# Optimization experiments

Measured on AMD Instinct MI355X. Metric: run time of the kernel, lower is better.

Reference implementation:

```python
import jax, jax.numpy as jnp
import numpy as np
import math

B, S, HID, NH = 64, 512, 256, 4
DH = HID // NH
EPS = 1e-12


def _dense(x, W, b):
    # torch nn.Linear: y = x @ W.T + b, W: [out, in]
    return jnp.einsum('bsi,oi->bso', x, W) + b


def _heads(x):
    # [B,S,HID] -> [B,NH,S,DH]
    return x.reshape(B, S, NH, DH).transpose(0, 2, 1, 3)


def _layernorm(x, w, b):
    u = jnp.mean(x, -1, keepdims=True)
    s = jnp.mean((x - u) ** 2, -1, keepdims=True)
    return w * ((x - u) / jnp.sqrt(s + EPS)) + b


def _wasserstein(mq, cq, mk, ck):
    # mean part: ||mq||^2 + ||mk||^2 - 2 mq.mk
    m_ret = (-2.0 * jnp.einsum('bhqd,bhkd->bhqk', mq, mk)
             + jnp.sum(mq ** 2, -1, keepdims=True)
             + jnp.sum(mk ** 2, -1, keepdims=True).swapaxes(-1, -2))
    sq, sk = jnp.sqrt(jnp.clip(cq, 1e-24)), jnp.sqrt(jnp.clip(ck, 1e-24))
    c_ret = (-2.0 * jnp.einsum('bhqd,bhkd->bhqk', sq, sk)
             + jnp.sum(cq, -1, keepdims=True)
             + jnp.sum(ck, -1, keepdims=True).swapaxes(-1, -2))
    return m_ret + c_ret


def setup_inputs() -> dict:
    key = jax.random.key(0)
    ks = jax.random.split(key, 16)
    inp = {
        'input_mean': jax.random.normal(ks[0], (B, S, HID), jnp.float32),
        'input_cov': jax.random.normal(ks[1], (B, S, HID), jnp.float32),
        'attention_mask': jnp.zeros((B, 1, S, S), jnp.float32),
    }
    sc = 1.0 / math.sqrt(HID)
    names = ['Wmq', 'Wmk', 'Wmv', 'Wcq', 'Wck', 'Wcv', 'Wmd', 'Wcd']
    for i, n in enumerate(names):
        inp[n] = jax.random.normal(ks[2 + i], (HID, HID), jnp.float32) * sc
        inp['b' + n[1:]] = jnp.zeros((HID,), jnp.float32)
    inp['ln_w'] = jnp.ones((HID,), jnp.float32)
    inp['ln_b'] = jnp.zeros((HID,), jnp.float32)
    return inp


def reference(input_mean, input_cov, attention_mask,
              Wmq, bmq, Wmk, bmk, Wmv, bmv,
              Wcq, bcq, Wck, bck, Wcv, bcv,
              Wmd, bmd, Wcd, bcd, ln_w, ln_b):
    mq = _heads(_dense(input_mean, Wmq, bmq))
    mk = _heads(_dense(input_mean, Wmk, bmk))
    mv = _heads(_dense(input_mean, Wmv, bmv))
    cq = _heads(jax.nn.elu(_dense(input_cov, Wcq, bcq)) + 1.0)
    ck = _heads(jax.nn.elu(_dense(input_cov, Wck, bck)) + 1.0)
    cv = _heads(jax.nn.elu(_dense(input_cov, Wcv, bcv)) + 1.0)

    dist = _wasserstein(mq, cq, mk, ck)            # [B,NH,S,S]
    scores = jnp.exp(-dist) / math.sqrt(DH) + attention_mask
    probs = jax.nn.softmax(scores, axis=-1)

    mean_ctx = jnp.einsum('bhqk,bhkd->bhqd', probs, mv)
    cov_ctx = jnp.einsum('bhqk,bhkd->bhqd', probs ** 2, cv)
    mean_ctx = mean_ctx.transpose(0, 2, 1, 3).reshape(B, S, HID)
    cov_ctx = cov_ctx.transpose(0, 2, 1, 3).reshape(B, S, HID)

    mean_h = _layernorm(_dense(mean_ctx, Wmd, bmd) + input_mean, ln_w, ln_b)
    cov_h = _layernorm(_dense(cov_ctx, Wcd, bcd) + input_cov, ln_w, ln_b)
    return mean_h, cov_h, probs
```

## Files before the change

### kernel.cpp

```cpp
#include <hip/hip_runtime.h>
#include <math.h>

#define B_    64
#define S_    512
#define HID_  256
#define NH_   4
#define DH_   64
#define BH_   (B_*NH_)
#define BS_   (B_*S_)
#define TSZ   (BH_*S_*DH_)
#define MEANH_ELEMS (BS_*HID_)
#define PROBS_OFF   (2*MEANH_ELEMS)

typedef __attribute__((ext_vector_type(8))) short s16x8;
typedef __attribute__((ext_vector_type(4))) short s16x4;
typedef __attribute__((ext_vector_type(4))) float f32x4;

#define MFMA16(acc, a, b) (acc) = __builtin_amdgcn_mfma_f32_16x16x32_bf16((a), (b), (acc), 0, 0, 0)

static __device__ __forceinline__ short f2bf(float f) {
    union { float f; unsigned u; } a; a.f = f;
    unsigned r = a.u + 0x7fffu + ((a.u >> 16) & 1u);
    return (short)(r >> 16);
}
static __device__ __forceinline__ float b2f(short s) {
    union { unsigned u; float f; } a; a.u = ((unsigned)(unsigned short)s) << 16;
    return a.f;
}

struct WSrc { const float* w[8]; };

__global__ __launch_bounds__(256) void k_w2bf(WSrc src, short* wbf) {
    int t  = blockIdx.x * 256 + threadIdx.x;
    int e4 = t * 4;
    int mi = e4 >> 16; int off = e4 & 65535;
    f32x4 v = *(const f32x4*)(src.w[mi] + off);
    s16x4 o;
    o[0] = f2bf(v[0]); o[1] = f2bf(v[1]); o[2] = f2bf(v[2]); o[3] = f2bf(v[3]);
    *(s16x4*)(wbf + mi * 65536 + off) = o;
}

struct BiasP { const float* b[6]; };

__global__ __launch_bounds__(256) void k_proj(const float* Xmean, const float* Xcov,
                                              const short* wbf, BiasP bp,
                                              short* mq, short* mk, short* sq, short* sk,
                                              short* mvT, short* cvT) {
    const int bz = blockIdx.z;
    const float* X = (bz < 3) ? Xmean : Xcov;
    const short* W = wbf + bz * 65536;
    const float* bias = bp.b[bz];
    const int m0 = blockIdx.x * 64, n0 = blockIdx.y * 64;
    const int tid = threadIdx.x, wv = tid >> 6, l = tid & 63;

    __shared__ __align__(16) short x_l[64][40];
    __shared__ __align__(16) short w_l[64][40];
    __shared__ __align__(16) short t_l[64][65];

    f32x4 zero4 = {0.f, 0.f, 0.f, 0.f};
    f32x4 acc[4] = {zero4, zero4, zero4, zero4};

    for (int kk = 0; kk < 8; kk++) {
        const int k0 = kk * 32;
        #pragma unroll
        for (int i = 0; i < 2; i++) {
            int g = tid + i * 256; int mr = g >> 3, ci = g & 7;
            f32x4 xv = *(const f32x4*)(X + (size_t)(m0 + mr) * HID_ + k0 + ci * 4);
            s16x4 xs; xs[0] = f2bf(xv[0]); xs[1] = f2bf(xv[1]); xs[2] = f2bf(xv[2]); xs[3] = f2bf(xv[3]);
            *(s16x4*)&x_l[mr][ci * 4] = xs;
        }
        {
            int o = tid >> 2, ci = tid & 3;
            *(s16x8*)&w_l[o][ci * 8] = *(const s16x8*)(W + (n0 + o) * HID_ + k0 + ci * 8);
        }
        __syncthreads();
        s16x8 a = *(const s16x8*)&x_l[wv * 16 + (l & 15)][8 * (l >> 4)];
        #pragma unroll
        for (int nt = 0; nt < 4; nt++) {
            s16x8 b = *(const s16x8*)&w_l[nt * 16 + (l & 15)][8 * (l >> 4)];
            MFMA16(acc[nt], a, b);
        }
        __syncthreads();
    }

    const bool tr = (bz == 2 || bz == 5);
    const int bb = m0 >> 9;
    const int s0 = m0 & 511;
    const int h  = blockIdx.y;
    short* dstd = (bz == 0) ? mq : (bz == 1) ? mk : (bz == 3) ? sq : sk;

    #pragma unroll
    for (int nt = 0; nt < 4; nt++) {
        #pragma unroll
        for (int r = 0; r < 4; r++) {
            int ml = wv * 16 + 4 * (l >> 4) + r;
            int ol = nt * 16 + (l & 15);
            float val = acc[nt][r] + bias[n0 + ol];
            if (bz == 3 || bz == 4) { float e1 = (val > 0.f) ? val + 1.f : __expf(val); val = sqrtf(fmaxf(e1, 1e-24f)); }
            else if (bz == 5)       { val = (val > 0.f) ? val + 1.f : __expf(val); }
            short bfv = f2bf(val);
            if (tr) t_l[ml][ol] = bfv;
            else    dstd[(((size_t)(bb * NH_ + h) * S_ + (s0 + ml)) * DH_) + ol] = bfv;
        }
    }
    if (tr) {
        __syncthreads();
        short* dst = (bz == 2) ? mvT : cvT;
        #pragma unroll
        for (int i = 0; i < 2; i++) {
            int g = tid + i * 256; int orow = g >> 3, ci = g & 7;
            s16x8 v;
            #pragma unroll
            for (int j = 0; j < 8; j++) v[j] = t_l[ci * 8 + j][orow];
            *(s16x8*)(dst + ((size_t)(bb * NH_ + h) * DH_ + orow) * S_ + s0 + ci * 8) = v;
        }
    }
}

__global__ __launch_bounds__(256) void k_rowsum(const short* mk, const short* sk, float* ksum) {
    int row = (blockIdx.x * 256 + threadIdx.x) >> 3;
    int c   = (threadIdx.x & 7) * 8;
    s16x8 av = *(const s16x8*)(mk + (size_t)row * 64 + c);
    s16x8 bv = *(const s16x8*)(sk + (size_t)row * 64 + c);
    float s = 0.f;
    #pragma unroll
    for (int j = 0; j < 8; j++) { float a = b2f(av[j]); float b = b2f(bv[j]); s += a * a + b * b; }
    #pragma unroll
    for (int m = 1; m < 8; m <<= 1) s += __shfl_xor(s, m);
    if ((threadIdx.x & 7) == 0) ksum[row] = s;
}

__global__ __launch_bounds__(256, 4) void k_attn(const short* mq, const short* mk,
                                                 const short* sq, const short* sk,
                                                 const short* mvT, const short* cvT,
                                                 const float* ksum,
                                                 const float* mask, float* probs,
                                                 short* mctx, short* cctx) {
    const int vb = (blockIdx.x & 7) * 512 + (blockIdx.x >> 3);
    const int bh = vb >> 4, qb = vb & 15;
    const int b = bh >> 2, h = bh & 3;
    const int q0 = qb * 32;
    const int tid = threadIdx.x, w = tid >> 6, l = tid & 63;
    const int mt = w & 1, kq = w >> 1;
    const int lg = l >> 4, lr = l & 15;

    __shared__ __align__(16) char smem[36864];
    __shared__ float rsum_l[32][2];
    short* s16p = (short*)smem;

#define KB(buf, t, row, col) (s16p + (((buf) * 2 + (t)) * 64 + (row)) * 72 + (col))
#define SWZ(row) ((((row) & 7) << 4) ^ (((row) & 8) << 3))

    const short* mkB = mk + (size_t)bh * (S_ * DH_);
    const short* skB = sk + (size_t)bh * (S_ * DH_);
    const float* ksB = ksum + bh * S_;
    const float* maskR = mask + (size_t)b * (S_ * S_) + (size_t)(q0 + mt * 16 + lr) * S_;

    const short* mqR = mq + (size_t)bh * (S_ * DH_) + (size_t)(q0 + mt * 16 + lr) * DH_;
    const short* sqR = sq + (size_t)bh * (S_ * DH_) + (size_t)(q0 + mt * 16 + lr) * DH_;
    s16x8 qm0 = *(const s16x8*)(mqR + 8 * lg);
    s16x8 qm1 = *(const s16x8*)(mqR + 32 + 8 * lg);
    s16x8 qv0 = *(const s16x8*)(sqR + 8 * lg);
    s16x8 qv1 = *(const s16x8*)(sqR + 32 + 8 * lg);
    float qsv = 0.f;
    #pragma unroll
    for (int j = 0; j < 8; j++) {
        float a0 = b2f(qm0[j]), a1 = b2f(qm1[j]);
        float c0 = b2f(qv0[j]), c1 = b2f(qv1[j]);
        qsv += a0 * a0 + a1 * a1 + c0 * c0 + c1 * c1;
    }
    qsv += __shfl_xor(qsv, 16); qsv += __shfl_xor(qsv, 32);

    const int srow = tid >> 3, sci = (tid & 7) * 8;
    s16x8 Rm[2], Rs[2];
    auto ldK = [&](int kt) {
        #pragma unroll
        for (int i = 0; i < 2; i++) {
            int row = kt * 64 + srow + i * 32;
            Rm[i] = *(const s16x8*)(mkB + row * 64 + sci);
            Rs[i] = *(const s16x8*)(skB + row * 64 + sci);
        }
    };
    auto wrK = [&](int buf) {
        #pragma unroll
        for (int i = 0; i < 2; i++) {
            *(s16x8*)KB(buf, 0, srow + i * 32, sci) = Rm[i];
            *(s16x8*)KB(buf, 1, srow + i * 32, sci) = Rs[i];
        }
    };

    ldK(0); wrK(0); ldK(1);
    __syncthreads();

    s16x4 pb[8][2];
    float rs = 0.f;
    #pragma unroll
    for (int kt = 0; kt < 8; kt++) {
        const int cb = kt & 1;
        #pragma unroll
        for (int nn = 0; nn < 2; nn++) {
            const int krl = kq * 32 + nn * 16 + lr;
            s16x8 am0 = *(const s16x8*)KB(cb, 0, krl, 8 * lg);
            s16x8 am1 = *(const s16x8*)KB(cb, 0, krl, 32 + 8 * lg);
            s16x8 as0 = *(const s16x8*)KB(cb, 1, krl, 8 * lg);
            s16x8 as1 = *(const s16x8*)KB(cb, 1, krl, 32 + 8 * lg);
            const int kbase = kt * 64 + kq * 32 + nn * 16 + 4 * lg;
            f32x4 kv  = *(const f32x4*)(ksB + kbase);
            f32x4 mkv = *(const f32x4*)(maskR + kbase);
            f32x4 acc = {0.f, 0.f, 0.f, 0.f};
            MFMA16(acc, am0, qm0); MFMA16(acc, am1, qm1);
            MFMA16(acc, as0, qv0); MFMA16(acc, as1, qv1);
            s16x4 pv;
            #pragma unroll
            for (int r = 0; r < 4; r++) {
                float dist = qsv + kv[r] - 2.f * acc[r];
                float t = __expf(-dist) * 0.125f;
                float p = __expf(t + mkv[r]);
                rs += p;
                pv[r] = f2bf(p);
            }
            pb[kt][nn] = pv;
        }
        if (kt < 7) {
            wrK(cb ^ 1);
            if (kt < 6) ldK(kt + 2);
        }
        __syncthreads();
    }

    rs += __shfl_xor(rs, 16); rs += __shfl_xor(rs, 32);
    if (l < 16) rsum_l[mt * 16 + l][kq] = rs;
    {
        const int wrow = mt * 16 + lr;
        const int sw = SWZ(wrow);
        #pragma unroll
        for (int kt = 0; kt < 8; kt++)
            #pragma unroll
            for (int nn = 0; nn < 2; nn++) {
                int colb = (kt * 64 + kq * 32 + nn * 16 + 4 * lg) * 2;
                *(s16x4*)(smem + wrow * 1024 + (colb ^ sw)) = pb[kt][nn];
            }
    }
    const short* mvR = mvT + (size_t)bh * (DH_ * S_) + (size_t)(w * 16 + lr) * S_;
    const short* cvR = cvT + (size_t)bh * (DH_ * S_) + (size_t)(w * 16 + lr) * S_;
    s16x8 Vbuf[2][4];
    auto LDV = [&](int kt, s16x8* V) {
        V[0] = *(const s16x8*)(mvR + kt * 64 + 8 * lg);
        V[1] = *(const s16x8*)(mvR + kt * 64 + 32 + 8 * lg);
        V[2] = *(const s16x8*)(cvR + kt * 64 + 8 * lg);
        V[3] = *(const s16x8*)(cvR + kt * 64 + 32 + 8 * lg);
    };
    LDV(0, Vbuf[0]);
    __syncthreads();

    {
        const int prow = tid >> 3, pc = tid & 7;
        const int sw = SWZ(prow);
        const float rvp = 1.f / (rsum_l[prow][0] + rsum_l[prow][1]);
        float* probsB = probs + (size_t)bh * (S_ * S_) + (size_t)(q0 + prow) * S_;
        #pragma unroll
        for (int i = 0; i < 8; i++) {
            int k0 = pc * 8 + i * 64;
            s16x8 pv = *(const s16x8*)(smem + prow * 1024 + ((k0 * 2) ^ sw));
            f32x4 o0, o1;
            #pragma unroll
            for (int j = 0; j < 4; j++) { o0[j] = b2f(pv[j]) * rvp; o1[j] = b2f(pv[4 + j]) * rvp; }
            *(f32x4*)(probsB + k0) = o0;
            *(f32x4*)(probsB + k0 + 4) = o1;
        }
    }

    float rvq[2];
    #pragma unroll
    for (int qt = 0; qt < 2; qt++)
        rvq[qt] = 1.f / (rsum_l[qt * 16 + lr][0] + rsum_l[qt * 16 + lr][1]);

    f32x4 zero4 = {0.f, 0.f, 0.f, 0.f};
    f32x4 om[2] = {zero4, zero4};
    f32x4 oc[2] = {zero4, zero4};
    #pragma unroll
    for (int kt = 0; kt < 8; kt++) {
        const int cur = kt & 1;
        if (kt < 7) LDV(kt + 1, Vbuf[cur ^ 1]);
        #pragma unroll
        for (int qt = 0; qt < 2; qt++) {
            const int brow = qt * 16 + lr;
            const int sw = SWZ(brow);
            #pragma unroll
            for (int koff = 0; koff < 2; koff++) {
                int byteoff = kt * 128 + koff * 64 + 16 * lg;
                s16x8 bp = *(const s16x8*)(smem + brow * 1024 + (byteoff ^ sw));
                s16x8 bp2;
                #pragma unroll
                for (int j = 0; j < 8; j++) { float f = b2f(bp[j]); bp2[j] = f2bf(f * f); }
                MFMA16(om[qt], Vbuf[cur][koff], bp);
                MFMA16(oc[qt], Vbuf[cur][2 + koff], bp2);
            }
        }
    }

    __syncthreads();
    char* cm = smem;
    char* cc = smem + 4096;
    #pragma unroll
    for (int qt = 0; qt < 2; qt++) {
        const int row = qt * 16 + lr;
        const int sw = SWZ(row);
        const float rv = rvq[qt];
        s16x4 vm, vc;
        #pragma unroll
        for (int r = 0; r < 4; r++) {
            vm[r] = f2bf(om[qt][r] * rv);
            vc[r] = f2bf(oc[qt][r] * rv * rv);
        }
        int colb = (w * 16 + 4 * lg) * 2;
        *(s16x4*)(cm + row * 128 + (colb ^ sw)) = vm;
        *(s16x4*)(cc + row * 128 + (colb ^ sw)) = vc;
    }
    __syncthreads();
    {
        const int row = tid >> 3, pc = tid & 7;
        const int sw = SWZ(row);
        s16x8 vm = *(const s16x8*)(cm + row * 128 + ((pc * 16) ^ sw));
        s16x8 vc = *(const s16x8*)(cc + row * 128 + ((pc * 16) ^ sw));
        size_t base = ((size_t)(b * S_ + q0 + row)) * HID_ + h * DH_ + pc * 8;
        *(s16x8*)(mctx + base) = vm;
        *(s16x8*)(cctx + base) = vc;
    }
#undef KB
#undef SWZ
}

__global__ __launch_bounds__(256) void k_final(const short* mctx, const short* cctx,
                                               const short* wbf,
                                               const float* bmd, const float* bcd,
                                               const float* Xmean, const float* Xcov,
                                               const float* lnw, const float* lnb,
                                               float* outbase) {
    const int which = blockIdx.y;
    const short* C = which ? cctx : mctx;
    const short* W = wbf + (6 + which) * 65536;
    const float* bias = which ? bcd : bmd;
    const float* X = which ? Xcov : Xmean;
    float* out = outbase + (size_t)which * MEANH_ELEMS;

    const int m0 = blockIdx.x * 32;
    const int tid = threadIdx.x, wv = tid >> 6, l = tid & 63;

    __shared__ __align__(16) short c_l[32][40];
    __shared__ __align__(16) short w_l[256][40];
    __shared__ float h_l[32][256];

    f32x4 zero4 = {0.f, 0.f, 0.f, 0.f};
    f32x4 acc[2][4];
    #pragma unroll
    for (int mtI = 0; mtI < 2; mtI++)
        #pragma unroll
        for (int nt = 0; nt < 4; nt++) acc[mtI][nt] = zero4;

    for (int kk = 0; kk < 8; kk++) {
        const int k0 = kk * 32;
        if (tid < 128) {
            int row = tid >> 2, ci = tid & 3;
            *(s16x8*)&c_l[row][ci * 8] = *(const s16x8*)(C + (size_t)(m0 + row) * HID_ + k0 + ci * 8);
        }
        #pragma unroll
        for (int i = 0; i < 4; i++) {
            int g = tid + i * 256; int o = g >> 2, ci = g & 3;
            *(s16x8*)&w_l[o][ci * 8] = *(const s16x8*)(W + o * HID_ + k0 + ci * 8);
        }
        __syncthreads();
        s16x8 a[2];
        #pragma unroll
        for (int mtI = 0; mtI < 2; mtI++)
            a[mtI] = *(const s16x8*)&c_l[mtI * 16 + (l & 15)][8 * (l >> 4)];
        #pragma unroll
        for (int nt = 0; nt < 4; nt++) {
            s16x8 bfr = *(const s16x8*)&w_l[wv * 64 + nt * 16 + (l & 15)][8 * (l >> 4)];
            MFMA16(acc[0][nt], a[0], bfr);
            MFMA16(acc[1][nt], a[1], bfr);
        }
        __syncthreads();
    }
    #pragma unroll
    for (int mtI = 0; mtI < 2; mtI++) {
        #pragma unroll
        for (int nt = 0; nt < 4; nt++) {
            #pragma unroll
            for (int r = 0; r < 4; r++) {
                int ml = mtI * 16 + 4 * (l >> 4) + r;
                int o = wv * 64 + nt * 16 + (l & 15);
                h_l[ml][o] = acc[mtI][nt][r] + bias[o] + X[(size_t)(m0 + ml) * HID_ + o];
            }
        }
    }
    __syncthreads();
    #pragma unroll
    for (int i = 0; i < 8; i++) {
        int row = wv * 8 + i;
        float s = 0.f;
        #pragma unroll
        for (int c = 0; c < 4; c++) s += h_l[row][l + c * 64];
        #pragma unroll
        for (int m = 1; m < 64; m <<= 1) s += __shfl_xor(s, m);
        float u = s * (1.f / 256.f);
        float s2 = 0.f;
        #pragma unroll
        for (int c = 0; c < 4; c++) { float d = h_l[row][l + c * 64] - u; s2 += d * d; }
        #pragma unroll
        for (int m = 1; m < 64; m <<= 1) s2 += __shfl_xor(s2, m);
        float rstd = rsqrtf(s2 * (1.f / 256.f) + 1e-12f);
        #pragma unroll
        for (int c = 0; c < 4; c++) {
            int o = l + c * 64;
            out[(size_t)(m0 + row) * HID_ + o] = lnw[o] * ((h_l[row][o] - u) * rstd) + lnb[o];
        }
    }
}

extern "C" void kernel_launch(void* const* d_in, const int* in_sizes, int n_in,
                              void* d_out, int out_size, void* d_ws, size_t ws_size,
                              hipStream_t stream) {
    const float* x_mean = (const float*)d_in[0];
    const float* x_cov  = (const float*)d_in[1];
    const float* mask   = (const float*)d_in[2];
    WSrc src;
    src.w[0] = (const float*)d_in[3];  src.w[1] = (const float*)d_in[5];
    src.w[2] = (const float*)d_in[7];  src.w[3] = (const float*)d_in[9];
    src.w[4] = (const float*)d_in[11]; src.w[5] = (const float*)d_in[13];
    src.w[6] = (const float*)d_in[15]; src.w[7] = (const float*)d_in[17];
    BiasP bp;
    bp.b[0] = (const float*)d_in[4];  bp.b[1] = (const float*)d_in[6];
    bp.b[2] = (const float*)d_in[8];  bp.b[3] = (const float*)d_in[10];
    bp.b[4] = (const float*)d_in[12]; bp.b[5] = (const float*)d_in[14];
    const float* bmd = (const float*)d_in[16];
    const float* bcd = (const float*)d_in[18];
    const float* lnw = (const float*)d_in[19];
    const float* lnb = (const float*)d_in[20];
    float* out = (float*)d_out;

    char* wsb = (char*)d_ws;
    short* wbf = (short*)wsb;
    short* mq  = (short*)(wsb + (1 << 20));
    short* mk  = mq  + TSZ;
    short* sq  = mk  + TSZ;
    short* sk  = sq  + TSZ;
    short* mvT = sk  + TSZ;
    short* cvT = mvT + TSZ;
    float* ksum = (float*)(cvT + TSZ);
    short* mctx = (short*)(ksum + (BH_ * S_));
    short* cctx = mctx + TSZ;

    float* probs = out + PROBS_OFF;

    hipLaunchKernelGGL(k_w2bf, dim3(512), dim3(256), 0, stream, src, wbf);
    hipLaunchKernelGGL(k_proj, dim3(512, 4, 6), dim3(256), 0, stream,
                       x_mean, x_cov, wbf, bp, mq, mk, sq, sk, mvT, cvT);
    hipLaunchKernelGGL(k_rowsum, dim3(4096), dim3(256), 0, stream, mk, sk, ksum);
    hipLaunchKernelGGL(k_attn, dim3(BH_ * 16), dim3(256), 0, stream,
                       mq, mk, sq, sk, mvT, cvT, ksum, mask, probs, mctx, cctx);
    hipLaunchKernelGGL(k_final, dim3(BS_ / 32, 2), dim3(256), 0, stream,
                       mctx, cctx, wbf, bmd, bcd, x_mean, x_cov, lnw, lnb, out);
}
```

Before: 373.2 us.

## Fuse row-norm sums into projection and restructure attention to keep probs in registers

```diff
diff --git a/kernel.cpp b/kernel.cpp
--- a/kernel.cpp
+++ b/kernel.cpp
@@ -9,6 +9,7 @@
 #define BH_   (B_*NH_)
 #define BS_   (B_*S_)
 #define TSZ   (BH_*S_*DH_)
+#define PSN   (BH_*S_)
 #define MEANH_ELEMS (BS_*HID_)
 #define PROBS_OFF   (2*MEANH_ELEMS)
 
@@ -26,6 +27,17 @@
 static __device__ __forceinline__ float b2f(short s) {
     union { unsigned u; float f; } a; a.u = ((unsigned)(unsigned short)s) << 16;
     return a.f;
+}
+static __device__ __forceinline__ unsigned cvt_pk_bf16(float a, float b) {
+    unsigned r;
+    asm("v_cvt_pk_bf16_f32 %0, %1, %2" : "=v"(r) : "v"(a), "v"(b));
+    return r;
+}
+static __device__ __forceinline__ void unpk2(int u, float& lo, float& hi) {
+    union { unsigned u; float f; } a, b;
+    a.u = ((unsigned)u) << 16;
+    b.u = ((unsigned)u) & 0xffff0000u;
+    lo = a.f; hi = b.f;
 }
 
 struct WSrc { const float* w[8]; };
@@ -45,7 +57,7 @@
 __global__ __launch_bounds__(256) void k_proj(const float* Xmean, const float* Xcov,
                                               const short* wbf, BiasP bp,
                                               short* mq, short* mk, short* sq, short* sk,
-                                              short* mvT, short* cvT) {
+                                              short* mvT, short* cvT, float* psums) {
     const int bz = blockIdx.z;
     const float* X = (bz < 3) ? Xmean : Xcov;
     const short* W = wbf + bz * 65536;
@@ -89,6 +101,8 @@
     const int h  = blockIdx.y;
     short* dstd = (bz == 0) ? mq : (bz == 1) ? mk : (bz == 3) ? sq : sk;
 
+    float ps[4] = {0.f, 0.f, 0.f, 0.f};
+
     #pragma unroll
     for (int nt = 0; nt < 4; nt++) {
         #pragma unroll
@@ -96,11 +110,33 @@
             int ml = wv * 16 + 4 * (l >> 4) + r;
             int ol = nt * 16 + (l & 15);
             float val = acc[nt][r] + bias[n0 + ol];
-            if (bz == 3 || bz == 4) { float e1 = (val > 0.f) ? val + 1.f : __expf(val); val = sqrtf(fmaxf(e1, 1e-24f)); }
-            else if (bz == 5)       { val = (val > 0.f) ? val + 1.f : __expf(val); }
+            if (bz == 3 || bz == 4) {
+                float e1 = (val > 0.f) ? val + 1.f : __expf(val);
+                e1 = fmaxf(e1, 1e-24f);
+                ps[r] += e1;
+                val = sqrtf(e1);
+            } else if (bz == 5) {
+                val = (val > 0.f) ? val + 1.f : __expf(val);
+            } else if (bz != 2) {
+                ps[r] += val * val;
+            }
             short bfv = f2bf(val);
             if (tr) t_l[ml][ol] = bfv;
             else    dstd[(((size_t)(bb * NH_ + h) * S_ + (s0 + ml)) * DH_) + ol] = bfv;
+        }
+    }
+    if (bz != 2 && bz != 5) {
+        const int aidx = (bz == 0) ? 0 : (bz == 1) ? 1 : (bz == 3) ? 2 : 3;
+        float* PS = psums + (size_t)aidx * PSN;
+        #pragma unroll
+        for (int r = 0; r < 4; r++) {
+            float s = ps[r];
+            s += __shfl_xor(s, 1); s += __shfl_xor(s, 2);
+            s += __shfl_xor(s, 4); s += __shfl_xor(s, 8);
+            if ((l & 15) == 0) {
+                int ml = wv * 16 + 4 * (l >> 4) + r;
+                PS[(size_t)(bb * NH_ + h) * S_ + (s0 + ml)] = s;
+            }
         }
     }
     if (tr) {
@@ -117,23 +153,10 @@
     }
 }
 
-__global__ __launch_bounds__(256) void k_rowsum(const short* mk, const short* sk, float* ksum) {
-    int row = (blockIdx.x * 256 + threadIdx.x) >> 3;
-    int c   = (threadIdx.x & 7) * 8;
-    s16x8 av = *(const s16x8*)(mk + (size_t)row * 64 + c);
-    s16x8 bv = *(const s16x8*)(sk + (size_t)row * 64 + c);
-    float s = 0.f;
-    #pragma unroll
-    for (int j = 0; j < 8; j++) { float a = b2f(av[j]); float b = b2f(bv[j]); s += a * a + b * b; }
-    #pragma unroll
-    for (int m = 1; m < 8; m <<= 1) s += __shfl_xor(s, m);
-    if ((threadIdx.x & 7) == 0) ksum[row] = s;
-}
-
 __global__ __launch_bounds__(256, 4) void k_attn(const short* mq, const short* mk,
                                                  const short* sq, const short* sk,
                                                  const short* mvT, const short* cvT,
-                                                 const float* ksum,
+                                                 const float* psums,
                                                  const float* mask, float* probs,
                                                  short* mctx, short* cctx) {
     const int vb = (blockIdx.x & 7) * 512 + (blockIdx.x >> 3);
@@ -144,191 +167,154 @@
     const int mt = w & 1, kq = w >> 1;
     const int lg = l >> 4, lr = l & 15;
 
-    __shared__ __align__(16) char smem[36864];
+    __shared__ __align__(16) float red[2][32][65];
+    __shared__ __align__(16) short obuf[2][32][72];
     __shared__ float rsum_l[32][2];
-    short* s16p = (short*)smem;
-
-#define KB(buf, t, row, col) (s16p + (((buf) * 2 + (t)) * 64 + (row)) * 72 + (col))
-#define SWZ(row) ((((row) & 7) << 4) ^ (((row) & 8) << 3))
-
-    const short* mkB = mk + (size_t)bh * (S_ * DH_);
-    const short* skB = sk + (size_t)bh * (S_ * DH_);
-    const float* ksB = ksum + bh * S_;
-    const float* maskR = mask + (size_t)b * (S_ * S_) + (size_t)(q0 + mt * 16 + lr) * S_;
-
-    const short* mqR = mq + (size_t)bh * (S_ * DH_) + (size_t)(q0 + mt * 16 + lr) * DH_;
-    const short* sqR = sq + (size_t)bh * (S_ * DH_) + (size_t)(q0 + mt * 16 + lr) * DH_;
+
+    const int qrow = q0 + mt * 16 + lr;
+    const size_t qoff = (size_t)bh * S_ + qrow;
+    const short* mqR = mq + qoff * DH_;
+    const short* sqR = sq + qoff * DH_;
     s16x8 qm0 = *(const s16x8*)(mqR + 8 * lg);
     s16x8 qm1 = *(const s16x8*)(mqR + 32 + 8 * lg);
     s16x8 qv0 = *(const s16x8*)(sqR + 8 * lg);
     s16x8 qv1 = *(const s16x8*)(sqR + 32 + 8 * lg);
-    float qsv = 0.f;
-    #pragma unroll
-    for (int j = 0; j < 8; j++) {
-        float a0 = b2f(qm0[j]), a1 = b2f(qm1[j]);
-        float c0 = b2f(qv0[j]), c1 = b2f(qv1[j]);
-        qsv += a0 * a0 + a1 * a1 + c0 * c0 + c1 * c1;
-    }
-    qsv += __shfl_xor(qsv, 16); qsv += __shfl_xor(qsv, 32);
-
-    const int srow = tid >> 3, sci = (tid & 7) * 8;
-    s16x8 Rm[2], Rs[2];
-    auto ldK = [&](int kt) {
-        #pragma unroll
-        for (int i = 0; i < 2; i++) {
-            int row = kt * 64 + srow + i * 32;
-            Rm[i] = *(const s16x8*)(mkB + row * 64 + sci);
-            Rs[i] = *(const s16x8*)(skB + row * 64 + sci);
-        }
-    };
-    auto wrK = [&](int buf) {
-        #pragma unroll
-        for (int i = 0; i < 2; i++) {
-            *(s16x8*)KB(buf, 0, srow + i * 32, sci) = Rm[i];
-            *(s16x8*)KB(buf, 1, srow + i * 32, sci) = Rs[i];
-        }
-    };
-
-    ldK(0); wrK(0); ldK(1);
-    __syncthreads();
+    const float qsv = psums[qoff] + psums[2 * (size_t)PSN + qoff];
+
+    const short* mkB = mk + (size_t)bh * (S_ * DH_);
+    const short* skB = sk + (size_t)bh * (S_ * DH_);
+    const float* ksMB = psums + 1 * (size_t)PSN + bh * S_;
+    const float* ksSB = psums + 3 * (size_t)PSN + bh * S_;
+    const float* maskR = mask + (size_t)b * (S_ * S_) + (size_t)qrow * S_;
 
     s16x4 pb[8][2];
     float rs = 0.f;
     #pragma unroll
     for (int kt = 0; kt < 8; kt++) {
-        const int cb = kt & 1;
         #pragma unroll
         for (int nn = 0; nn < 2; nn++) {
-            const int krl = kq * 32 + nn * 16 + lr;
-            s16x8 am0 = *(const s16x8*)KB(cb, 0, krl, 8 * lg);
-            s16x8 am1 = *(const s16x8*)KB(cb, 0, krl, 32 + 8 * lg);
-            s16x8 as0 = *(const s16x8*)KB(cb, 1, krl, 8 * lg);
-            s16x8 as1 = *(const s16x8*)KB(cb, 1, krl, 32 + 8 * lg);
+            const int krl = kt * 64 + kq * 32 + nn * 16 + lr;
+            const short* kmp = mkB + krl * 64;
+            const short* ksp = skB + krl * 64;
+            s16x8 am0 = *(const s16x8*)(kmp + 8 * lg);
+            s16x8 am1 = *(const s16x8*)(kmp + 32 + 8 * lg);
+            s16x8 as0 = *(const s16x8*)(ksp + 8 * lg);
+            s16x8 as1 = *(const s16x8*)(ksp + 32 + 8 * lg);
             const int kbase = kt * 64 + kq * 32 + nn * 16 + 4 * lg;
-            f32x4 kv  = *(const f32x4*)(ksB + kbase);
+            f32x4 kvM = *(const f32x4*)(ksMB + kbase);
+            f32x4 kvS = *(const f32x4*)(ksSB + kbase);
             f32x4 mkv = *(const f32x4*)(maskR + kbase);
             f32x4 acc = {0.f, 0.f, 0.f, 0.f};
             MFMA16(acc, am0, qm0); MFMA16(acc, am1, qm1);
             MFMA16(acc, as0, qv0); MFMA16(acc, as1, qv1);
-            s16x4 pv;
+            float p[4];
             #pragma unroll
             for (int r = 0; r < 4; r++) {
-                float dist = qsv + kv[r] - 2.f * acc[r];
+                float kvq = qsv + kvM[r] + kvS[r];
+                float dist = kvq - 2.f * acc[r];
                 float t = __expf(-dist) * 0.125f;
-                float p = __expf(t + mkv[r]);
-                rs += p;
-                pv[r] = f2bf(p);
-            }
-            pb[kt][nn] = pv;
-        }
-        if (kt < 7) {
-            wrK(cb ^ 1);
-            if (kt < 6) ldK(kt + 2);
-        }
-        __syncthreads();
+                float pp = __expf(t + mkv[r]);
+                rs += pp; p[r] = pp;
+            }
+            union { unsigned u[2]; s16x4 v; } pk;
+            pk.u[0] = cvt_pk_bf16(p[0], p[1]);
+            pk.u[1] = cvt_pk_bf16(p[2], p[3]);
+            pb[kt][nn] = pk.v;
+        }
     }
 
     rs += __shfl_xor(rs, 16); rs += __shfl_xor(rs, 32);
     if (l < 16) rsum_l[mt * 16 + l][kq] = rs;
-    {
-        const int wrow = mt * 16 + lr;
-        const int sw = SWZ(wrow);
-        #pragma unroll
-        for (int kt = 0; kt < 8; kt++)
+    __syncthreads();
+    const float rvp = 1.f / (rsum_l[mt * 16 + lr][0] + rsum_l[mt * 16 + lr][1]);
+
+    const int src0 = ((lg & 1) * 32 + lr) * 4;
+    const int src1 = src0 + 64;
+    const bool hi = (l & 32) != 0;
+    const short* mvB = mvT + (size_t)bh * (DH_ * S_);
+    const short* cvB = cvT + (size_t)bh * (DH_ * S_);
+    float* probsR = probs + (size_t)bh * (S_ * S_) + (size_t)qrow * S_ + kq * 32 + 8 * lg;
+
+    f32x4 zero4 = {0.f, 0.f, 0.f, 0.f};
+    f32x4 cm[4] = {zero4, zero4, zero4, zero4};
+    f32x4 cc[4] = {zero4, zero4, zero4, zero4};
+
+    #pragma unroll
+    for (int kt = 0; kt < 8; kt++) {
+        union { s16x4 v; int i[2]; } p0, p1;
+        p0.v = pb[kt][0]; p1.v = pb[kt][1];
+        int b00 = __builtin_amdgcn_ds_bpermute(src0, p0.i[0]);
+        int b01 = __builtin_amdgcn_ds_bpermute(src0, p0.i[1]);
+        int b10 = __builtin_amdgcn_ds_bpermute(src0, p1.i[0]);
+        int b11 = __builtin_amdgcn_ds_bpermute(src0, p1.i[1]);
+        int c00 = __builtin_amdgcn_ds_bpermute(src1, p0.i[0]);
+        int c01 = __builtin_amdgcn_ds_bpermute(src1, p0.i[1]);
+        int c10 = __builtin_amdgcn_ds_bpermute(src1, p1.i[0]);
+        int c11 = __builtin_amdgcn_ds_bpermute(src1, p1.i[1]);
+        union { int i[4]; s16x8 v; } af, af2;
+        af.i[0] = hi ? b10 : b00;
+        af.i[1] = hi ? b11 : b01;
+        af.i[2] = hi ? c10 : c00;
+        af.i[3] = hi ? c11 : c01;
+
+        float f0,f1,f2,f3,f4,f5,f6,f7;
+        unpk2(af.i[0], f0, f1); unpk2(af.i[1], f2, f3);
+        unpk2(af.i[2], f4, f5); unpk2(af.i[3], f6, f7);
+
+        f32x4 o0 = {f0 * rvp, f1 * rvp, f2 * rvp, f3 * rvp};
+        f32x4 o1 = {f4 * rvp, f5 * rvp, f6 * rvp, f7 * rvp};
+        *(f32x4*)(probsR + kt * 64)     = o0;
+        *(f32x4*)(probsR + kt * 64 + 4) = o1;
+
+        af2.i[0] = (int)cvt_pk_bf16(f0 * f0, f1 * f1);
+        af2.i[1] = (int)cvt_pk_bf16(f2 * f2, f3 * f3);
+        af2.i[2] = (int)cvt_pk_bf16(f4 * f4, f5 * f5);
+        af2.i[3] = (int)cvt_pk_bf16(f6 * f6, f7 * f7);
+
+        const int kb2 = kt * 64 + kq * 32 + 8 * lg;
+        #pragma unroll
+        for (int dt = 0; dt < 4; dt++) {
+            const size_t boff = (size_t)(dt * 16 + lr) * S_ + kb2;
+            s16x8 bm = *(const s16x8*)(mvB + boff);
+            s16x8 bc = *(const s16x8*)(cvB + boff);
+            MFMA16(cm[dt], af.v, bm);
+            MFMA16(cc[dt], af2.v, bc);
+        }
+    }
+
+    if (kq == 0) {
+        #pragma unroll
+        for (int dt = 0; dt < 4; dt++)
             #pragma unroll
-            for (int nn = 0; nn < 2; nn++) {
-                int colb = (kt * 64 + kq * 32 + nn * 16 + 4 * lg) * 2;
-                *(s16x4*)(smem + wrow * 1024 + (colb ^ sw)) = pb[kt][nn];
-            }
-    }
-    const short* mvR = mvT + (size_t)bh * (DH_ * S_) + (size_t)(w * 16 + lr) * S_;
-    const short* cvR = cvT + (size_t)bh * (DH_ * S_) + (size_t)(w * 16 + lr) * S_;
-    s16x8 Vbuf[2][4];
-    auto LDV = [&](int kt, s16x8* V) {
-        V[0] = *(const s16x8*)(mvR + kt * 64 + 8 * lg);
-        V[1] = *(const s16x8*)(mvR + kt * 64 + 32 + 8 * lg);
-        V[2] = *(const s16x8*)(cvR + kt * 64 + 8 * lg);
-        V[3] = *(const s16x8*)(cvR + kt * 64 + 32 + 8 * lg);
-    };
-    LDV(0, Vbuf[0]);
+            for (int r = 0; r < 4; r++) {
+                red[0][mt * 16 + 4 * lg + r][dt * 16 + lr] = cm[dt][r];
+                red[1][mt * 16 + 4 * lg + r][dt * 16 + lr] = cc[dt][r];
+            }
+    }
     __syncthreads();
-
-    {
-        const int prow = tid >> 3, pc = tid & 7;
-        const int sw = SWZ(prow);
-        const float rvp = 1.f / (rsum_l[prow][0] + rsum_l[prow][1]);
-        float* probsB = probs + (size_t)bh * (S_ * S_) + (size_t)(q0 + prow) * S_;
-        #pragma unroll
-        for (int i = 0; i < 8; i++) {
-            int k0 = pc * 8 + i * 64;
-            s16x8 pv = *(const s16x8*)(smem + prow * 1024 + ((k0 * 2) ^ sw));
-            f32x4 o0, o1;
+    if (kq == 1) {
+        #pragma unroll
+        for (int r = 0; r < 4; r++) {
+            const int row = mt * 16 + 4 * lg + r;
+            const float rv = 1.f / (rsum_l[row][0] + rsum_l[row][1]);
             #pragma unroll
-            for (int j = 0; j < 4; j++) { o0[j] = b2f(pv[j]) * rvp; o1[j] = b2f(pv[4 + j]) * rvp; }
-            *(f32x4*)(probsB + k0) = o0;
-            *(f32x4*)(probsB + k0 + 4) = o1;
-        }
-    }
-
-    float rvq[2];
-    #pragma unroll
-    for (int qt = 0; qt < 2; qt++)
-        rvq[qt] = 1.f / (rsum_l[qt * 16 + lr][0] + rsum_l[qt * 16 + lr][1]);
-
-    f32x4 zero4 = {0.f, 0.f, 0.f, 0.f};
-    f32x4 om[2] = {zero4, zero4};
-    f32x4 oc[2] = {zero4, zero4};
-    #pragma unroll
-    for (int kt = 0; kt < 8; kt++) {
-        const int cur = kt & 1;
-        if (kt < 7) LDV(kt + 1, Vbuf[cur ^ 1]);
-        #pragma unroll
-        for (int qt = 0; qt < 2; qt++) {
-            const int brow = qt * 16 + lr;
-            const int sw = SWZ(brow);
-            #pragma unroll
-            for (int koff = 0; koff < 2; koff++) {
-                int byteoff = kt * 128 + koff * 64 + 16 * lg;
-                s16x8 bp = *(const s16x8*)(smem + brow * 1024 + (byteoff ^ sw));
-                s16x8 bp2;
-                #pragma unroll
-                for (int j = 0; j < 8; j++) { float f = b2f(bp[j]); bp2[j] = f2bf(f * f); }
-                MFMA16(om[qt], Vbuf[cur][koff], bp);
-                MFMA16(oc[qt], Vbuf[cur][2 + koff], bp2);
-            }
-        }
-    }
-
-    __syncthreads();
-    char* cm = smem;
-    char* cc = smem + 4096;
-    #pragma unroll
-    for (int qt = 0; qt < 2; qt++) {
-        const int row = qt * 16 + lr;
-        const int sw = SWZ(row);
-        const float rv = rvq[qt];
-        s16x4 vm, vc;
-        #pragma unroll
-        for (int r = 0; r < 4; r++) {
-            vm[r] = f2bf(om[qt][r] * rv);
-            vc[r] = f2bf(oc[qt][r] * rv * rv);
-        }
-        int colb = (w * 16 + 4 * lg) * 2;
-        *(s16x4*)(cm + row * 128 + (colb ^ sw)) = vm;
-        *(s16x4*)(cc + row * 128 + (colb ^ sw)) = vc;
+            for (int dt = 0; dt < 4; dt++) {
+                float vm = (red[0][row][dt * 16 + lr] + cm[dt][r]) * rv;
+                float vc = (red[1][row][dt * 16 + lr] + cc[dt][r]) * rv * rv;
+                obuf[0][row][dt * 16 + lr] = f2bf(vm);
+                obuf[1][row][dt * 16 + lr] = f2bf(vc);
+            }
+        }
     }
     __syncthreads();
     {
         const int row = tid >> 3, pc = tid & 7;
-        const int sw = SWZ(row);
-        s16x8 vm = *(const s16x8*)(cm + row * 128 + ((pc * 16) ^ sw));
-        s16x8 vc = *(const s16x8*)(cc + row * 128 + ((pc * 16) ^ sw));
+        s16x8 vm = *(const s16x8*)&obuf[0][row][pc * 8];
+        s16x8 vc = *(const s16x8*)&obuf[1][row][pc * 8];
         size_t base = ((size_t)(b * S_ + q0 + row)) * HID_ + h * DH_ + pc * 8;
         *(s16x8*)(mctx + base) = vm;
         *(s16x8*)(cctx + base) = vc;
     }
-#undef KB
-#undef SWZ
 }
 
 __global__ __launch_bounds__(256) void k_final(const short* mctx, const short* cctx,
@@ -447,18 +433,17 @@
     short* sk  = sq  + TSZ;
     short* mvT = sk  + TSZ;
     short* cvT = mvT + TSZ;
-    float* ksum = (float*)(cvT + TSZ);
-    short* mctx = (short*)(ksum + (BH_ * S_));
+    float* psums = (float*)(cvT + TSZ);
+    short* mctx = (short*)(psums + 4 * (size_t)PSN);
     short* cctx = mctx + TSZ;
 
     float* probs = out + PROBS_OFF;
 
     hipLaunchKernelGGL(k_w2bf, dim3(512), dim3(256), 0, stream, src, wbf);
     hipLaunchKernelGGL(k_proj, dim3(512, 4, 6), dim3(256), 0, stream,
-                       x_mean, x_cov, wbf, bp, mq, mk, sq, sk, mvT, cvT);
-    hipLaunchKernelGGL(k_rowsum, dim3(4096), dim3(256), 0, stream, mk, sk, ksum);
+                       x_mean, x_cov, wbf, bp, mq, mk, sq, sk, mvT, cvT, psums);
     hipLaunchKernelGGL(k_attn, dim3(BH_ * 16), dim3(256), 0, stream,
-                       mq, mk, sq, sk, mvT, cvT, ksum, mask, probs, mctx, cctx);
+                       mq, mk, sq, sk, mvT, cvT, psums, mask, probs, mctx, cctx);
     hipLaunchKernelGGL(k_final, dim3(BS_ / 32, 2), dim3(256), 0, stream,
                        mctx, cctx, wbf, bmd, bcd, x_mean, x_cov, lnw, lnb, out);
 }
```

Result: slower. 490.6 us (+31.4%).

## Fuse row squared-norm sums into projection epilogue, drop rowsum kernel

Applied to the files above, without the earlier changes.

```diff
diff --git a/kernel.cpp b/kernel.cpp
--- a/kernel.cpp
+++ b/kernel.cpp
@@ -9,6 +9,7 @@
 #define BH_   (B_*NH_)
 #define BS_   (B_*S_)
 #define TSZ   (BH_*S_*DH_)
+#define PSN   (BH_*S_)
 #define MEANH_ELEMS (BS_*HID_)
 #define PROBS_OFF   (2*MEANH_ELEMS)
 
@@ -26,6 +27,17 @@
 static __device__ __forceinline__ float b2f(short s) {
     union { unsigned u; float f; } a; a.u = ((unsigned)(unsigned short)s) << 16;
     return a.f;
+}
+static __device__ __forceinline__ unsigned cvt_pk_bf16(float a, float b) {
+    unsigned r;
+    asm("v_cvt_pk_bf16_f32 %0, %1, %2" : "=v"(r) : "v"(a), "v"(b));
+    return r;
+}
+static __device__ __forceinline__ void unpk2(int u, float& lo, float& hi) {
+    union { unsigned u; float f; } a, b;
+    a.u = ((unsigned)u) << 16;
+    b.u = ((unsigned)u) & 0xffff0000u;
+    lo = a.f; hi = b.f;
 }
 
 struct WSrc { const float* w[8]; };
@@ -45,7 +57,7 @@
 __global__ __launch_bounds__(256) void k_proj(const float* Xmean, const float* Xcov,
                                               const short* wbf, BiasP bp,
                                               short* mq, short* mk, short* sq, short* sk,
-                                              short* mvT, short* cvT) {
+                                              short* mvT, short* cvT, float* psums) {
     const int bz = blockIdx.z;
     const float* X = (bz < 3) ? Xmean : Xcov;
     const short* W = wbf + bz * 65536;
@@ -89,6 +101,8 @@
     const int h  = blockIdx.y;
     short* dstd = (bz == 0) ? mq : (bz == 1) ? mk : (bz == 3) ? sq : sk;
 
+    float ps[4] = {0.f, 0.f, 0.f, 0.f};
+
     #pragma unroll
     for (int nt = 0; nt < 4; nt++) {
         #pragma unroll
@@ -96,11 +110,33 @@
             int ml = wv * 16 + 4 * (l >> 4) + r;
             int ol = nt * 16 + (l & 15);
             float val = acc[nt][r] + bias[n0 + ol];
-            if (bz == 3 || bz == 4) { float e1 = (val > 0.f) ? val + 1.f : __expf(val); val = sqrtf(fmaxf(e1, 1e-24f)); }
-            else if (bz == 5)       { val = (val > 0.f) ? val + 1.f : __expf(val); }
+            if (bz == 3 || bz == 4) {
+                float e1 = (val > 0.f) ? val + 1.f : __expf(val);
+                val = sqrtf(fmaxf(e1, 1e-24f));
+            } else if (bz == 5) {
+                val = (val > 0.f) ? val + 1.f : __expf(val);
+            }
             short bfv = f2bf(val);
+            if (bz == 0 || bz == 1 || bz == 3 || bz == 4) {
+                float qv = b2f(bfv);
+                ps[r] += qv * qv;
+            }
             if (tr) t_l[ml][ol] = bfv;
             else    dstd[(((size_t)(bb * NH_ + h) * S_ + (s0 + ml)) * DH_) + ol] = bfv;
+        }
+    }
+    if (bz != 2 && bz != 5) {
+        const int aidx = (bz == 0) ? 0 : (bz == 1) ? 1 : (bz == 3) ? 2 : 3;
+        float* PS = psums + (size_t)aidx * PSN;
+        #pragma unroll
+        for (int r = 0; r < 4; r++) {
+            float s = ps[r];
+            s += __shfl_xor(s, 1); s += __shfl_xor(s, 2);
+            s += __shfl_xor(s, 4); s += __shfl_xor(s, 8);
+            if ((l & 15) == 0) {
+                int ml = wv * 16 + 4 * (l >> 4) + r;
+                PS[(size_t)(bb * NH_ + h) * S_ + (s0 + ml)] = s;
+            }
         }
     }
     if (tr) {
@@ -117,23 +153,10 @@
     }
 }
 
-__global__ __launch_bounds__(256) void k_rowsum(const short* mk, const short* sk, float* ksum) {
-    int row = (blockIdx.x * 256 + threadIdx.x) >> 3;
-    int c   = (threadIdx.x & 7) * 8;
-    s16x8 av = *(const s16x8*)(mk + (size_t)row * 64 + c);
-    s16x8 bv = *(const s16x8*)(sk + (size_t)row * 64 + c);
-    float s = 0.f;
-    #pragma unroll
-    for (int j = 0; j < 8; j++) { float a = b2f(av[j]); float b = b2f(bv[j]); s += a * a + b * b; }
-    #pragma unroll
-    for (int m = 1; m < 8; m <<= 1) s += __shfl_xor(s, m);
-    if ((threadIdx.x & 7) == 0) ksum[row] = s;
-}
-
 __global__ __launch_bounds__(256, 4) void k_attn(const short* mq, const short* mk,
                                                  const short* sq, const short* sk,
                                                  const short* mvT, const short* cvT,
-                                                 const float* ksum,
+                                                 const float* psums,
                                                  const float* mask, float* probs,
                                                  short* mctx, short* cctx) {
     const int vb = (blockIdx.x & 7) * 512 + (blockIdx.x >> 3);
@@ -153,23 +176,18 @@
 
     const short* mkB = mk + (size_t)bh * (S_ * DH_);
     const short* skB = sk + (size_t)bh * (S_ * DH_);
-    const float* ksB = ksum + bh * S_;
+    const float* ksMB = psums + 1 * (size_t)PSN + bh * S_;
+    const float* ksSB = psums + 3 * (size_t)PSN + bh * S_;
     const float* maskR = mask + (size_t)b * (S_ * S_) + (size_t)(q0 + mt * 16 + lr) * S_;
 
-    const short* mqR = mq + (size_t)bh * (S_ * DH_) + (size_t)(q0 + mt * 16 + lr) * DH_;
-    const short* sqR = sq + (size_t)bh * (S_ * DH_) + (size_t)(q0 + mt * 16 + lr) * DH_;
+    const size_t qoff = (size_t)bh * S_ + (q0 + mt * 16 + lr);
+    const short* mqR = mq + qoff * DH_;
+    const short* sqR = sq + qoff * DH_;
     s16x8 qm0 = *(const s16x8*)(mqR + 8 * lg);
     s16x8 qm1 = *(const s16x8*)(mqR + 32 + 8 * lg);
     s16x8 qv0 = *(const s16x8*)(sqR + 8 * lg);
     s16x8 qv1 = *(const s16x8*)(sqR + 32 + 8 * lg);
-    float qsv = 0.f;
-    #pragma unroll
-    for (int j = 0; j < 8; j++) {
-        float a0 = b2f(qm0[j]), a1 = b2f(qm1[j]);
-        float c0 = b2f(qv0[j]), c1 = b2f(qv1[j]);
-        qsv += a0 * a0 + a1 * a1 + c0 * c0 + c1 * c1;
-    }
-    qsv += __shfl_xor(qsv, 16); qsv += __shfl_xor(qsv, 32);
+    const float qsv = psums[qoff] + psums[2 * (size_t)PSN + qoff];
 
     const int srow = tid >> 3, sci = (tid & 7) * 8;
     s16x8 Rm[2], Rs[2];
@@ -205,7 +223,8 @@
             s16x8 as0 = *(const s16x8*)KB(cb, 1, krl, 8 * lg);
             s16x8 as1 = *(const s16x8*)KB(cb, 1, krl, 32 + 8 * lg);
             const int kbase = kt * 64 + kq * 32 + nn * 16 + 4 * lg;
-            f32x4 kv  = *(const f32x4*)(ksB + kbase);
+            f32x4 kvM = *(const f32x4*)(ksMB + kbase);
+            f32x4 kvS = *(const f32x4*)(ksSB + kbase);
             f32x4 mkv = *(const f32x4*)(maskR + kbase);
             f32x4 acc = {0.f, 0.f, 0.f, 0.f};
             MFMA16(acc, am0, qm0); MFMA16(acc, am1, qm1);
@@ -213,7 +232,7 @@
             s16x4 pv;
             #pragma unroll
             for (int r = 0; r < 4; r++) {
-                float dist = qsv + kv[r] - 2.f * acc[r];
+                float dist = qsv + kvM[r] + kvS[r] - 2.f * acc[r];
                 float t = __expf(-dist) * 0.125f;
                 float p = __expf(t + mkv[r]);
                 rs += p;
@@ -289,12 +308,17 @@
             #pragma unroll
             for (int koff = 0; koff < 2; koff++) {
                 int byteoff = kt * 128 + koff * 64 + 16 * lg;
-                s16x8 bp = *(const s16x8*)(smem + brow * 1024 + (byteoff ^ sw));
-                s16x8 bp2;
-                #pragma unroll
-                for (int j = 0; j < 8; j++) { float f = b2f(bp[j]); bp2[j] = f2bf(f * f); }
-                MFMA16(om[qt], Vbuf[cur][koff], bp);
-                MFMA16(oc[qt], Vbuf[cur][2 + koff], bp2);
+                union { int i[4]; s16x8 v; } bp, bp2;
+                bp.v = *(const s16x8*)(smem + brow * 1024 + (byteoff ^ sw));
+                float f0, f1, f2, f3, f4, f5, f6, f7;
+                unpk2(bp.i[0], f0, f1); unpk2(bp.i[1], f2, f3);
+                unpk2(bp.i[2], f4, f5); unpk2(bp.i[3], f6, f7);
+                bp2.i[0] = (int)cvt_pk_bf16(f0 * f0, f1 * f1);
+                bp2.i[1] = (int)cvt_pk_bf16(f2 * f2, f3 * f3);
+                bp2.i[2] = (int)cvt_pk_bf16(f4 * f4, f5 * f5);
+                bp2.i[3] = (int)cvt_pk_bf16(f6 * f6, f7 * f7);
+                MFMA16(om[qt], Vbuf[cur][koff], bp.v);
+                MFMA16(oc[qt], Vbuf[cur][2 + koff], bp2.v);
             }
         }
     }
@@ -447,18 +471,17 @@
     short* sk  = sq  + TSZ;
     short* mvT = sk  + TSZ;
     short* cvT = mvT + TSZ;
-    float* ksum = (float*)(cvT + TSZ);
-    short* mctx = (short*)(ksum + (BH_ * S_));
+    float* psums = (float*)(cvT + TSZ);
+    short* mctx = (short*)(psums + 4 * (size_t)PSN);
     short* cctx = mctx + TSZ;
 
     float* probs = out + PROBS_OFF;
 
     hipLaunchKernelGGL(k_w2bf, dim3(512), dim3(256), 0, stream, src, wbf);
     hipLaunchKernelGGL(k_proj, dim3(512, 4, 6), dim3(256), 0, stream,
-                       x_mean, x_cov, wbf, bp, mq, mk, sq, sk, mvT, cvT);
-    hipLaunchKernelGGL(k_rowsum, dim3(4096), dim3(256), 0, stream, mk, sk, ksum);
+                       x_mean, x_cov, wbf, bp, mq, mk, sq, sk, mvT, cvT, psums);
     hipLaunchKernelGGL(k_attn, dim3(BH_ * 16), dim3(256), 0, stream,
-                       mq, mk, sq, sk, mvT, cvT, ksum, mask, probs, mctx, cctx);
+                       mq, mk, sq, sk, mvT, cvT, psums, mask, probs, mctx, cctx);
     hipLaunchKernelGGL(k_final, dim3(BS_ / 32, 2), dim3(256), 0, stream,
                        mctx, cctx, wbf, bmd, bcd, x_mean, x_cov, lnw, lnb, out);
 }
```

Result: slower. 388.3 us (+4.0%).
